# Kernel tuning notes

Hardware: AMD Instinct MI355X
Metric: run time of the kernel (lower is better)

## Reference

```python
import jax, jax.numpy as jnp
import numpy as np

TEMPERATURE = 1.0
EPS = 1e-7
MAX_NORM = 0.9  # project points strictly inside the Poincare ball


def _project_ball(x):
    n = jnp.linalg.norm(x, axis=-1, keepdims=True)
    return x * jnp.minimum(1.0, MAX_NORM / jnp.maximum(n, EPS))


def setup_inputs() -> dict:
    key = jax.random.key(0)
    kq, kk, kv = jax.random.split(key, 3)
    B, Nq, Nk, D, V = 8, 2048, 2048, 64, 128
    queries = _project_ball(jax.random.normal(kq, (B, Nq, D), dtype=jnp.float32))
    keys = _project_ball(jax.random.normal(kk, (B, Nk, D), dtype=jnp.float32))
    values = jax.random.normal(kv, (B, Nk, V), dtype=jnp.float32)
    return {"queries": queries, "keys": keys, "values": values}


def _poincare_pairwise_dist(x, y):
    # x: (B,N,D), y: (B,M,D) -> (B,N,M) geodesic distances on the Poincare ball
    x2 = jnp.sum(x * x, axis=-1)            # (B,N)
    y2 = jnp.sum(y * y, axis=-1)            # (B,M)
    xy = jnp.einsum('bnd,bmd->bnm', x, y)   # (B,N,M)
    sq = jnp.maximum(x2[:, :, None] + y2[:, None, :] - 2.0 * xy, 0.0)
    denom = jnp.maximum((1.0 - x2)[:, :, None] * (1.0 - y2)[:, None, :], EPS)
    arg = 1.0 + 2.0 * sq / denom
    return jnp.arccosh(jnp.maximum(arg, 1.0 + EPS))


def reference(queries, keys, values):
    distances = _poincare_pairwise_dist(queries, keys)          # (B,Nq,Nk)
    scores = -(distances * distances) / TEMPERATURE
    attention_weights = jax.nn.softmax(scores, axis=-1)         # (B,Nq,Nk)
    output = jnp.einsum('bnm,bmv->bnv', attention_weights, values)  # (B,Nq,V)
    return output, attention_weights
```

## Files before the change

kernel.cpp:

```cpp
#include <hip/hip_runtime.h>
#include <math.h>

#define BB 8
#define NQ 2048
#define NK 2048
#define DD 64
#define VV 128
#define EPSF 1e-7f
#define NT3 (NK / 64)
#define FIXROWS 1024

typedef _Float16 half_t;
typedef half_t half8 __attribute__((ext_vector_type(8)));
typedef float  floatx4 __attribute__((ext_vector_type(4)));

__device__ __forceinline__ float score_exp(float x2, float y2, float xy)
{
    float px = 1.f - x2, py = 1.f - y2;
    float sq = fmaxf(x2 + y2 - 2.f * xy, 0.f);
    float dn = fmaxf(px * py, EPSF);
    float tt = fmaxf(2.f * sq * __builtin_amdgcn_rcpf(dn), EPSF);
    float u  = tt + __builtin_amdgcn_sqrtf(fmaf(tt, tt, tt + tt));
    float d  = __logf(1.f + u);
    return __expf(-d * d);
}

__device__ __forceinline__ half8 cvt8(float4 a, float4 b)
{
    half8 h;
    h[0] = (half_t)a.x; h[1] = (half_t)a.y; h[2] = (half_t)a.z; h[3] = (half_t)a.w;
    h[4] = (half_t)b.x; h[5] = (half_t)b.y; h[6] = (half_t)b.z; h[7] = (half_t)b.w;
    return h;
}

__device__ __forceinline__ size_t khg_idx(int b, int tile, int f, int l)
{ return (((size_t)b * NT3 + tile) * 8 + f) * 64 + l; }
__device__ __forceinline__ size_t vhg_idx(int b, int tile, int f, int l)
{ return (((size_t)b * NT3 + tile) * 16 + f) * 64 + l; }

__device__ __forceinline__ int ssh_byte(int row, int col)
{
    return ((row << 7) + (col << 1)) ^ ((row & 7) << 4);
}

__global__ __launch_bounds__(256)
void k0_prep(const float* __restrict__ Q, const float* __restrict__ Kp,
             const float* __restrict__ V, half8* __restrict__ Khg,
             half8* __restrict__ Vhg, float* __restrict__ y2g,
             float* __restrict__ x2g)
{
    __shared__ float sVt[64 * VV];

    const int t = threadIdx.x, b = blockIdx.y, tile = blockIdx.x;
    const int kt = tile * 64;
    const float* Kb = Kp + (size_t)b * NK * DD;
    const float* Qb = Q  + (size_t)b * NQ * DD;
    const float* Vb = V  + (size_t)b * NK * VV;

#pragma unroll
    for (int i = 0; i < 8; ++i)
        ((float4*)sVt)[t + i * 256] = ((const float4*)(Vb + (size_t)kt * VV))[t + i * 256];

#pragma unroll
    for (int i = 0; i < 2; ++i) {
        int s = t + i * 256, f = s >> 6, l = s & 63;
        int krow = kt + (f >> 1) * 16 + (l & 15);
        int dcol = (f & 1) * 32 + (l >> 4) * 8;
        const float4* kp = (const float4*)(Kb + (size_t)krow * DD + dcol);
        Khg[khg_idx(b, tile, f, l)] = cvt8(kp[0], kp[1]);
    }
    if (t < 64) {
        const float4* kr = (const float4*)(Kb + (size_t)(kt + t) * DD);
        float s = 0.f;
#pragma unroll
        for (int i = 0; i < 16; ++i) {
            float4 v = kr[i];
            s = fmaf(v.x,v.x,s); s = fmaf(v.y,v.y,s);
            s = fmaf(v.z,v.z,s); s = fmaf(v.w,v.w,s);
        }
        y2g[(size_t)b * NK + kt + t] = s;
    } else if (t < 128) {
        int r = t - 64;
        const float4* qr = (const float4*)(Qb + (size_t)(kt + r) * DD);
        float s = 0.f;
#pragma unroll
        for (int i = 0; i < 16; ++i) {
            float4 v = qr[i];
            s = fmaf(v.x,v.x,s); s = fmaf(v.y,v.y,s);
            s = fmaf(v.z,v.z,s); s = fmaf(v.w,v.w,s);
        }
        x2g[(size_t)b * NQ + kt + r] = s;
    }
    __syncthreads();

#pragma unroll
    for (int i = 0; i < 4; ++i) {
        int s = t + i * 256, f = s >> 6, l = s & 63;
        int krow_l = (f & 1) * 32 + (l >> 4) * 8;
        int vcol   = (f >> 1) * 16 + (l & 15);
        half8 h;
#pragma unroll
        for (int j = 0; j < 8; ++j) h[j] = (half_t)sVt[(krow_l + j) * VV + vcol];
        Vhg[vhg_idx(b, tile, f, l)] = h;
    }
}

__global__ __launch_bounds__(256)
void k_main(const float* __restrict__ Q, const half8* __restrict__ Khg,
            const half8* __restrict__ Vhg, const float* __restrict__ y2g,
            const float* __restrict__ x2g, float* __restrict__ W,
            float* __restrict__ O, float* __restrict__ RS)
{
    __shared__ half_t sSh[32 * 64];
    __shared__ float  y2k[NK];
    __shared__ float  part[2][32];
    __shared__ float  rsumS[32];

    const int t = threadIdx.x, w = t >> 6, lane = t & 63;
    const int n = lane & 15, quad = lane >> 4;
    const int qh = w & 1, kh = w >> 1;

    const int bid = blockIdx.x;
    const int swz = (bid & 7) * 64 + (bid >> 3);
    const int b = swz >> 6, qb = (swz & 63) * 32;
    const bool wskip = (b == 0) && (qb < FIXROWS);

    const float* Qb = Q + (size_t)b * NQ * DD;

#pragma unroll
    for (int i = 0; i < 2; ++i)
        ((float4*)y2k)[t + i * 256] = ((const float4*)(y2g + (size_t)b * NK))[t + i * 256];

    half8 af[2];
#pragma unroll
    for (int ds = 0; ds < 2; ++ds) {
        const float4* qp = (const float4*)(Qb + (size_t)(qb + qh*16 + n) * DD + ds*32 + quad*8);
        af[ds] = cvt8(qp[0], qp[1]);
    }
    float x2r[4];
#pragma unroll
    for (int r = 0; r < 4; ++r)
        x2r[r] = x2g[(size_t)b * NQ + qb + qh * 16 + quad * 4 + r];
    __syncthreads();

    const int khbase = kh * 1024;
    float srow[4] = {0.f, 0.f, 0.f, 0.f};

    half8 bf[8];
#pragma unroll
    for (int f = 0; f < 8; ++f) bf[f] = Khg[khg_idx(b, kh * 16, f, lane)];

#pragma unroll 1
    for (int kt0 = 0; kt0 < 1024; kt0 += 64) {
        const bool pf = (kt0 + 64) < 1024;
        half8 bfn[8];
        if (pf) {
#pragma unroll
            for (int f = 0; f < 8; ++f)
                bfn[f] = Khg[khg_idx(b, kh * 16 + ((kt0 + 64) >> 6), f, lane)];
        }

        floatx4 acc4[4] = {};
#pragma unroll
        for (int nt = 0; nt < 4; ++nt)
#pragma unroll
            for (int ds = 0; ds < 2; ++ds)
                acc4[nt] = __builtin_amdgcn_mfma_f32_16x16x32_f16(
                    af[ds], bf[nt * 2 + ds], acc4[nt], 0, 0, 0);

#pragma unroll
        for (int nt = 0; nt < 4; ++nt) {
            int lcol = khbase + kt0 + nt * 16 + n;
            float y2 = y2k[lcol];
#pragma unroll
            for (int r = 0; r < 4; ++r)
                srow[r] += score_exp(x2r[r], y2, acc4[nt][r]);
        }
        if (pf) {
#pragma unroll
            for (int f = 0; f < 8; ++f) bf[f] = bfn[f];
        }
    }

#pragma unroll
    for (int off = 1; off < 16; off <<= 1)
#pragma unroll
        for (int r = 0; r < 4; ++r) srow[r] += __shfl_xor(srow[r], off);
    if (n == 0)
#pragma unroll
        for (int r = 0; r < 4; ++r) part[kh][qh * 16 + quad * 4 + r] = srow[r];
    __syncthreads();
    if (t < 32) {
        float s = part[0][t] + part[1][t];
        RS[(size_t)b * NQ + qb + t] = s;
        rsumS[t] = s;
    }
    __syncthreads();

    float rlr[4];
#pragma unroll
    for (int r = 0; r < 4; ++r)
        rlr[r] = __builtin_amdgcn_rcpf(rsumS[qh * 16 + quad * 4 + r]);

    float* Wb = W + (size_t)b * NQ * NK;
    floatx4 acc[4] = {};

    half8 kf[4];
#pragma unroll
    for (int i = 0; i < 4; ++i) kf[i] = Khg[khg_idx(b, 0, kh * 4 + i, lane)];

#pragma unroll 1
    for (int tt = 0; tt < NT3; ++tt) {
        const bool pf = (tt + 1) < NT3;

        floatx4 a2[2] = {};
#pragma unroll
        for (int nt = 0; nt < 2; ++nt)
#pragma unroll
            for (int ds = 0; ds < 2; ++ds)
                a2[nt] = __builtin_amdgcn_mfma_f32_16x16x32_f16(
                    af[ds], kf[nt * 2 + ds], a2[nt], 0, 0, 0);

        half8 vf[8];
#pragma unroll
        for (int i = 0; i < 8; ++i) vf[i] = Vhg[vhg_idx(b, tt, kh * 8 + i, lane)];
        half8 kfn[4];
        if (pf) {
#pragma unroll
            for (int i = 0; i < 4; ++i) kfn[i] = Khg[khg_idx(b, tt + 1, kh * 4 + i, lane)];
        }

#pragma unroll
        for (int nt = 0; nt < 2; ++nt) {
            int col = kh * 32 + nt * 16 + n;
            int gcol = tt * 64 + col;
            float y2 = y2k[gcol];
#pragma unroll
            for (int r = 0; r < 4; ++r) {
                float e  = score_exp(x2r[r], y2, a2[nt][r]);
                float wv = e * rlr[r];
                int row = qh * 16 + quad * 4 + r;
                if (!wskip)
                    __builtin_nontemporal_store(wv, Wb + (size_t)(qb + row) * NK + gcol);
                *(half_t*)((char*)sSh + ssh_byte(row, col)) = (half_t)wv;
            }
        }
        __syncthreads();

        const int row2 = qh * 16 + n;
        half8 a0 = *(const half8*)((const char*)sSh + ssh_byte(row2, quad * 8));
        half8 a1 = *(const half8*)((const char*)sSh + ssh_byte(row2, 32 + quad * 8));
#pragma unroll
        for (int nt = 0; nt < 4; ++nt) {
            acc[nt] = __builtin_amdgcn_mfma_f32_16x16x32_f16(
                a0, vf[nt * 2 + 0], acc[nt], 0, 0, 0);
            acc[nt] = __builtin_amdgcn_mfma_f32_16x16x32_f16(
                a1, vf[nt * 2 + 1], acc[nt], 0, 0, 0);
        }
        __syncthreads();

        if (pf) {
#pragma unroll
            for (int i = 0; i < 4; ++i) kf[i] = kfn[i];
        }
    }

    float* Ob = O + (size_t)b * NQ * VV;
#pragma unroll
    for (int nt = 0; nt < 4; ++nt)
#pragma unroll
        for (int r = 0; r < 4; ++r)
            Ob[(size_t)(qb + qh * 16 + quad * 4 + r) * VV + kh * 64 + nt * 16 + n]
                = acc[nt][r];
}

__global__ __launch_bounds__(256)
void k4_wfix(const float* __restrict__ Q, const float* __restrict__ Kp,
             const float* __restrict__ RS, float* __restrict__ W)
{
    __shared__ half8 sB[8 * 64];
    __shared__ float y2k[256];
    __shared__ float x2q[32];

    const int t = threadIdx.x, w = t >> 6, lane = t & 63;
    const int n = lane & 15, quad = lane >> 4;
    const int qh = w & 1, kn = w >> 1;
    const int qb = blockIdx.x * 32;
    const int kz = blockIdx.y * 256;

    {
        const float4* kr = (const float4*)(Kp + (size_t)(kz + t) * DD);
        float s = 0.f;
#pragma unroll
        for (int i = 0; i < 16; ++i) {
            float4 v = kr[i];
            s = fmaf(v.x,v.x,s); s = fmaf(v.y,v.y,s);
            s = fmaf(v.z,v.z,s); s = fmaf(v.w,v.w,s);
        }
        y2k[t] = s;
    }
    if (t < 32) {
        const float4* qr = (const float4*)(Q + (size_t)(qb + t) * DD);
        float s = 0.f;
#pragma unroll
        for (int i = 0; i < 16; ++i) {
            float4 v = qr[i];
            s = fmaf(v.x,v.x,s); s = fmaf(v.y,v.y,s);
            s = fmaf(v.z,v.z,s); s = fmaf(v.w,v.w,s);
        }
        x2q[t] = s;
    }
    __syncthreads();

    half8 af[2];
#pragma unroll
    for (int ds = 0; ds < 2; ++ds) {
        const float4* qp = (const float4*)(Q + (size_t)(qb + qh*16 + n) * DD + ds*32 + quad*8);
        af[ds] = cvt8(qp[0], qp[1]);
    }
    float x2r[4], rlr[4];
#pragma unroll
    for (int r = 0; r < 4; ++r) {
        int row = qb + qh * 16 + quad * 4 + r;
        x2r[r] = x2q[qh * 16 + quad * 4 + r];
        rlr[r] = __builtin_amdgcn_rcpf(RS[row]);
    }

#pragma unroll 1
    for (int kt = 0; kt < 256; kt += 64) {
        __syncthreads();
#pragma unroll
        for (int i = 0; i < 2; ++i) {
            int s = t + i * 256, f = s >> 6, l = s & 63;
            int krow = kz + kt + (f >> 1) * 16 + (l & 15);
            int dcol = (f & 1) * 32 + (l >> 4) * 8;
            const float4* kp = (const float4*)(Kp + (size_t)krow * DD + dcol);
            sB[f * 64 + l] = cvt8(kp[0], kp[1]);
        }
        __syncthreads();

        floatx4 a2[2] = {};
#pragma unroll
        for (int nt = 0; nt < 2; ++nt)
#pragma unroll
            for (int ds = 0; ds < 2; ++ds)
                a2[nt] = __builtin_amdgcn_mfma_f32_16x16x32_f16(
                    af[ds], sB[((kn * 2 + nt) * 2 + ds) * 64 + lane], a2[nt], 0, 0, 0);

#pragma unroll
        for (int nt = 0; nt < 2; ++nt) {
            int col = kn * 32 + nt * 16 + n;
            float y2 = y2k[kt + col];
#pragma unroll
            for (int r = 0; r < 4; ++r) {
                float e = score_exp(x2r[r], y2, a2[nt][r]);
                int row = qh * 16 + quad * 4 + r;
                W[(size_t)(qb + row) * NK + kz + kt + col] = e * rlr[r];
            }
        }
    }
}

extern "C" void kernel_launch(void* const* d_in, const int* in_sizes, int n_in,
                              void* d_out, int out_size, void* d_ws, size_t ws_size,
                              hipStream_t stream)
{
    const float* Q  = (const float*)d_in[0];
    const float* Kp = (const float*)d_in[1];
    const float* Vp = (const float*)d_in[2];

    float* O     = (float*)d_out;
    float* attnW = O + (size_t)BB * NQ * VV;

    half8* Khg = (half8*)attnW;
    half8* Vhg = Khg + (size_t)BB * NT3 * 8 * 64;
    float* y2g = (float*)(Vhg + (size_t)BB * NT3 * 16 * 64);
    float* x2g = y2g + (size_t)BB * NK;

    float* RS = (float*)d_ws;

    k0_prep<<<dim3(NK / 64, BB),     256, 0, stream>>>(Q, Kp, Vp, Khg, Vhg, y2g, x2g);
    k_main <<<dim3(BB * (NQ / 32)),  256, 0, stream>>>(Q, Khg, Vhg, y2g, x2g, attnW, O, RS);
    k4_wfix<<<dim3(FIXROWS / 32, 8), 256, 0, stream>>>(Q, Kp, RS, attnW);
}
```

Before: 244.5 us.

## Double k_main waves per block, use exp2/log2 scoring, cache norms for fixup

```diff
diff --git a/kernel.cpp b/kernel.cpp
--- a/kernel.cpp
+++ b/kernel.cpp
@@ -16,13 +16,12 @@
 
 __device__ __forceinline__ float score_exp(float x2, float y2, float xy)
 {
-    float px = 1.f - x2, py = 1.f - y2;
-    float sq = fmaxf(x2 + y2 - 2.f * xy, 0.f);
-    float dn = fmaxf(px * py, EPSF);
+    float sq = fmaf(-2.f, xy, x2 + y2);
+    float dn = fmaxf((1.f - x2) * (1.f - y2), EPSF);
     float tt = fmaxf(2.f * sq * __builtin_amdgcn_rcpf(dn), EPSF);
     float u  = tt + __builtin_amdgcn_sqrtf(fmaf(tt, tt, tt + tt));
-    float d  = __logf(1.f + u);
-    return __expf(-d * d);
+    float L  = __log2f(1.f + u);
+    return __builtin_amdgcn_exp2f(-0.6931471805599453f * L * L);
 }
 
 __device__ __forceinline__ half8 cvt8(float4 a, float4 b)
@@ -47,7 +46,8 @@
 void k0_prep(const float* __restrict__ Q, const float* __restrict__ Kp,
              const float* __restrict__ V, half8* __restrict__ Khg,
              half8* __restrict__ Vhg, float* __restrict__ y2g,
-             float* __restrict__ x2g)
+             float* __restrict__ x2g, float* __restrict__ wsY,
+             float* __restrict__ wsX)
 {
     __shared__ float sVt[64 * VV];
 
@@ -79,6 +79,7 @@
             s = fmaf(v.z,v.z,s); s = fmaf(v.w,v.w,s);
         }
         y2g[(size_t)b * NK + kt + t] = s;
+        if (b == 0) wsY[kt + t] = s;
     } else if (t < 128) {
         int r = t - 64;
         const float4* qr = (const float4*)(Qb + (size_t)(kt + r) * DD);
@@ -90,6 +91,7 @@
             s = fmaf(v.z,v.z,s); s = fmaf(v.w,v.w,s);
         }
         x2g[(size_t)b * NQ + kt + r] = s;
+        if (b == 0) wsX[kt + r] = s;
     }
     __syncthreads();
 
@@ -105,7 +107,7 @@
     }
 }
 
-__global__ __launch_bounds__(256)
+__global__ __launch_bounds__(512, 4)
 void k_main(const float* __restrict__ Q, const half8* __restrict__ Khg,
             const half8* __restrict__ Vhg, const float* __restrict__ y2g,
             const float* __restrict__ x2g, float* __restrict__ W,
@@ -113,12 +115,12 @@
 {
     __shared__ half_t sSh[32 * 64];
     __shared__ float  y2k[NK];
-    __shared__ float  part[2][32];
+    __shared__ float  part[4][32];
     __shared__ float  rsumS[32];
 
     const int t = threadIdx.x, w = t >> 6, lane = t & 63;
     const int n = lane & 15, quad = lane >> 4;
-    const int qh = w & 1, kh = w >> 1;
+    const int qh = w & 1, kq = w >> 1;
 
     const int bid = blockIdx.x;
     const int swz = (bid & 7) * 64 + (bid >> 3);
@@ -127,9 +129,7 @@
 
     const float* Qb = Q + (size_t)b * NQ * DD;
 
-#pragma unroll
-    for (int i = 0; i < 2; ++i)
-        ((float4*)y2k)[t + i * 256] = ((const float4*)(y2g + (size_t)b * NK))[t + i * 256];
+    ((float4*)y2k)[t] = ((const float4*)(y2g + (size_t)b * NK))[t];
 
     half8 af[2];
 #pragma unroll
@@ -143,21 +143,20 @@
         x2r[r] = x2g[(size_t)b * NQ + qb + qh * 16 + quad * 4 + r];
     __syncthreads();
 
-    const int khbase = kh * 1024;
     float srow[4] = {0.f, 0.f, 0.f, 0.f};
 
     half8 bf[8];
 #pragma unroll
-    for (int f = 0; f < 8; ++f) bf[f] = Khg[khg_idx(b, kh * 16, f, lane)];
+    for (int f = 0; f < 8; ++f) bf[f] = Khg[khg_idx(b, kq * 8, f, lane)];
 
 #pragma unroll 1
-    for (int kt0 = 0; kt0 < 1024; kt0 += 64) {
-        const bool pf = (kt0 + 64) < 1024;
+    for (int kt0 = 0; kt0 < 512; kt0 += 64) {
+        const bool pf = (kt0 + 64) < 512;
         half8 bfn[8];
         if (pf) {
 #pragma unroll
             for (int f = 0; f < 8; ++f)
-                bfn[f] = Khg[khg_idx(b, kh * 16 + ((kt0 + 64) >> 6), f, lane)];
+                bfn[f] = Khg[khg_idx(b, kq * 8 + ((kt0 + 64) >> 6), f, lane)];
         }
 
         floatx4 acc4[4] = {};
@@ -170,7 +169,7 @@
 
 #pragma unroll
         for (int nt = 0; nt < 4; ++nt) {
-            int lcol = khbase + kt0 + nt * 16 + n;
+            int lcol = kq * 512 + kt0 + nt * 16 + n;
             float y2 = y2k[lcol];
 #pragma unroll
             for (int r = 0; r < 4; ++r)
@@ -188,10 +187,10 @@
         for (int r = 0; r < 4; ++r) srow[r] += __shfl_xor(srow[r], off);
     if (n == 0)
 #pragma unroll
-        for (int r = 0; r < 4; ++r) part[kh][qh * 16 + quad * 4 + r] = srow[r];
+        for (int r = 0; r < 4; ++r) part[kq][qh * 16 + quad * 4 + r] = srow[r];
     __syncthreads();
     if (t < 32) {
-        float s = part[0][t] + part[1][t];
+        float s = (part[0][t] + part[1][t]) + (part[2][t] + part[3][t]);
         RS[(size_t)b * NQ + qb + t] = s;
         rsumS[t] = s;
     }
@@ -203,41 +202,39 @@
         rlr[r] = __builtin_amdgcn_rcpf(rsumS[qh * 16 + quad * 4 + r]);
 
     float* Wb = W + (size_t)b * NQ * NK;
-    floatx4 acc[4] = {};
-
-    half8 kf[4];
-#pragma unroll
-    for (int i = 0; i < 4; ++i) kf[i] = Khg[khg_idx(b, 0, kh * 4 + i, lane)];
+    floatx4 acc[2] = {};
+
+    half8 kf[2];
+#pragma unroll
+    for (int ds = 0; ds < 2; ++ds) kf[ds] = Khg[khg_idx(b, 0, kq * 2 + ds, lane)];
 
 #pragma unroll 1
     for (int tt = 0; tt < NT3; ++tt) {
         const bool pf = (tt + 1) < NT3;
 
-        floatx4 a2[2] = {};
-#pragma unroll
-        for (int nt = 0; nt < 2; ++nt)
+        floatx4 a2 = {};
+        a2 = __builtin_amdgcn_mfma_f32_16x16x32_f16(af[0], kf[0], a2, 0, 0, 0);
+        a2 = __builtin_amdgcn_mfma_f32_16x16x32_f16(af[1], kf[1], a2, 0, 0, 0);
+
+        half8 vf[4];
+        vf[0] = Vhg[vhg_idx(b, tt, kq * 2,           lane)];
+        vf[1] = Vhg[vhg_idx(b, tt, kq * 2 + 1,       lane)];
+        vf[2] = Vhg[vhg_idx(b, tt, (kq + 4) * 2,     lane)];
+        vf[3] = Vhg[vhg_idx(b, tt, (kq + 4) * 2 + 1, lane)];
+        half8 kfn[2];
+        if (pf) {
 #pragma unroll
             for (int ds = 0; ds < 2; ++ds)
-                a2[nt] = __builtin_amdgcn_mfma_f32_16x16x32_f16(
-                    af[ds], kf[nt * 2 + ds], a2[nt], 0, 0, 0);
-
-        half8 vf[8];
-#pragma unroll
-        for (int i = 0; i < 8; ++i) vf[i] = Vhg[vhg_idx(b, tt, kh * 8 + i, lane)];
-        half8 kfn[4];
-        if (pf) {
-#pragma unroll
-            for (int i = 0; i < 4; ++i) kfn[i] = Khg[khg_idx(b, tt + 1, kh * 4 + i, lane)];
-        }
-
-#pragma unroll
-        for (int nt = 0; nt < 2; ++nt) {
-            int col = kh * 32 + nt * 16 + n;
+                kfn[ds] = Khg[khg_idx(b, tt + 1, kq * 2 + ds, lane)];
+        }
+
+        {
+            int col  = kq * 16 + n;
             int gcol = tt * 64 + col;
             float y2 = y2k[gcol];
 #pragma unroll
             for (int r = 0; r < 4; ++r) {
-                float e  = score_exp(x2r[r], y2, a2[nt][r]);
+                float e  = score_exp(x2r[r], y2, a2[r]);
                 float wv = e * rlr[r];
                 int row = qh * 16 + quad * 4 + r;
                 if (!wskip)
@@ -250,66 +247,43 @@
         const int row2 = qh * 16 + n;
         half8 a0 = *(const half8*)((const char*)sSh + ssh_byte(row2, quad * 8));
         half8 a1 = *(const half8*)((const char*)sSh + ssh_byte(row2, 32 + quad * 8));
-#pragma unroll
-        for (int nt = 0; nt < 4; ++nt) {
-            acc[nt] = __builtin_amdgcn_mfma_f32_16x16x32_f16(
-                a0, vf[nt * 2 + 0], acc[nt], 0, 0, 0);
-            acc[nt] = __builtin_amdgcn_mfma_f32_16x16x32_f16(
-                a1, vf[nt * 2 + 1], acc[nt], 0, 0, 0);
-        }
+        acc[0] = __builtin_amdgcn_mfma_f32_16x16x32_f16(a0, vf[0], acc[0], 0, 0, 0);
+        acc[0] = __builtin_amdgcn_mfma_f32_16x16x32_f16(a1, vf[1], acc[0], 0, 0, 0);
+        acc[1] = __builtin_amdgcn_mfma_f32_16x16x32_f16(a0, vf[2], acc[1], 0, 0, 0);
+        acc[1] = __builtin_amdgcn_mfma_f32_16x16x32_f16(a1, vf[3], acc[1], 0, 0, 0);
         __syncthreads();
 
-        if (pf) {
-#pragma unroll
-            for (int i = 0; i < 4; ++i) kf[i] = kfn[i];
-        }
+        if (pf) { kf[0] = kfn[0]; kf[1] = kfn[1]; }
     }
 
     float* Ob = O + (size_t)b * NQ * VV;
 #pragma unroll
-    for (int nt = 0; nt < 4; ++nt)
+    for (int ci = 0; ci < 2; ++ci) {
+        int c = kq + ci * 4;
 #pragma unroll
         for (int r = 0; r < 4; ++r)
-            Ob[(size_t)(qb + qh * 16 + quad * 4 + r) * VV + kh * 64 + nt * 16 + n]
-                = acc[nt][r];
+            Ob[(size_t)(qb + qh * 16 + quad * 4 + r) * VV + c * 16 + n]
+                = acc[ci][r];
+    }
 }
 
 __global__ __launch_bounds__(256)
 void k4_wfix(const float* __restrict__ Q, const float* __restrict__ Kp,
-             const float* __restrict__ RS, float* __restrict__ W)
+             const float* __restrict__ RS, const float* __restrict__ wsY,
+             const float* __restrict__ wsX, float* __restrict__ W)
 {
     __shared__ half8 sB[8 * 64];
-    __shared__ float y2k[256];
+    __shared__ float y2k[128];
     __shared__ float x2q[32];
 
     const int t = threadIdx.x, w = t >> 6, lane = t & 63;
     const int n = lane & 15, quad = lane >> 4;
     const int qh = w & 1, kn = w >> 1;
     const int qb = blockIdx.x * 32;
-    const int kz = blockIdx.y * 256;
-
-    {
-        const float4* kr = (const float4*)(Kp + (size_t)(kz + t) * DD);
-        float s = 0.f;
-#pragma unroll
-        for (int i = 0; i < 16; ++i) {
-            float4 v = kr[i];
-            s = fmaf(v.x,v.x,s); s = fmaf(v.y,v.y,s);
-            s = fmaf(v.z,v.z,s); s = fmaf(v.w,v.w,s);
-        }
-        y2k[t] = s;
-    }
-    if (t < 32) {
-        const float4* qr = (const float4*)(Q + (size_t)(qb + t) * DD);
-        float s = 0.f;
-#pragma unroll
-        for (int i = 0; i < 16; ++i) {
-            float4 v = qr[i];
-            s = fmaf(v.x,v.x,s); s = fmaf(v.y,v.y,s);
-            s = fmaf(v.z,v.z,s); s = fmaf(v.w,v.w,s);
-        }
-        x2q[t] = s;
-    }
+    const int kz = blockIdx.y * 128;
+
+    if (t < 128) y2k[t] = wsY[kz + t];
+    if (t < 32)  x2q[t] = wsX[qb + t];
     __syncthreads();
 
     half8 af[2];
@@ -327,7 +301,7 @@
     }
 
 #pragma unroll 1
-    for (int kt = 0; kt < 256; kt += 64) {
+    for (int kt = 0; kt < 128; kt += 64) {
         __syncthreads();
 #pragma unroll
         for (int i = 0; i < 2; ++i) {
@@ -377,9 +351,11 @@
     float* y2g = (float*)(Vhg + (size_t)BB * NT3 * 16 * 64);
     float* x2g = y2g + (size_t)BB * NK;
 
-    float* RS = (float*)d_ws;
-
-    k0_prep<<<dim3(NK / 64, BB),     256, 0, stream>>>(Q, Kp, Vp, Khg, Vhg, y2g, x2g);
-    k_main <<<dim3(BB * (NQ / 32)),  256, 0, stream>>>(Q, Khg, Vhg, y2g, x2g, attnW, O, RS);
-    k4_wfix<<<dim3(FIXROWS / 32, 8), 256, 0, stream>>>(Q, Kp, RS, attnW);
-}
+    float* RS  = (float*)d_ws;
+    float* wsY = RS  + (size_t)BB * NQ;
+    float* wsX = wsY + NK;
+
+    k0_prep<<<dim3(NK / 64, BB),      256, 0, stream>>>(Q, Kp, Vp, Khg, Vhg, y2g, x2g, wsY, wsX);
+    k_main <<<dim3(BB * (NQ / 32)),   512, 0, stream>>>(Q, Khg, Vhg, y2g, x2g, attnW, O, RS);
+    k4_wfix<<<dim3(FIXROWS / 32, 16), 256, 0, stream>>>(Q, Kp, RS, wsY, wsX, attnW);
+}
```

Measured after the change: 209.7 us. -14.2%, faster.
